# Kernel optimization log

Hardware: AMD Instinct MI355X
Metric: run time of the kernel (lower is better)

Reference implementation:

```python
import jax, jax.numpy as jnp
import numpy as np

E, H, I, T = 8, 2048, 1024, 16384  # experts, hidden, moe_intermediate, total tokens


def setup_inputs() -> dict:
    key = jax.random.key(0)
    k1, k2, k3, k4 = jax.random.split(key, 4)
    hidden_states = jax.random.normal(k1, (T, H), dtype=jnp.float32)
    # ragged per-expert token counts, summing exactly to T (tokens pre-sorted by expert)
    group_sizes = jnp.array([1024, 3072, 2048, 4096, 512, 1536, 2560, 1536], dtype=jnp.int32)
    std = 0.01  # nn.initializers.normal() default stddev
    gate_w = jax.random.normal(k2, (E, H, I), dtype=jnp.float32) * std
    up_w = jax.random.normal(k3, (E, H, I), dtype=jnp.float32) * std
    down_w = jax.random.normal(k4, (E, I, H), dtype=jnp.float32) * std
    return {"hidden_states": hidden_states, "gate_w": gate_w, "up_w": up_w,
            "down_w": down_w, "group_sizes": group_sizes}


def reference(hidden_states, gate_w, up_w, down_w, group_sizes):
    # grouped GEMM: rows of hidden_states are contiguous per-expert blocks of
    # sizes group_sizes[e]; each block is multiplied by that expert's kernel.
    g = jax.lax.ragged_dot(hidden_states, gate_w, group_sizes)   # [T, I]
    u = jax.lax.ragged_dot(hidden_states, up_w, group_sizes)     # [T, I]
    h = jax.nn.silu(g) * u                                       # SwiGLU gating
    return jax.lax.ragged_dot(h, down_w, group_sizes)            # [T, H]
```

## Files before the change

kernel.cpp:

```cpp
#include <hip/hip_runtime.h>
#include <hip/hip_bf16.h>

#define E_ 8
#define H_ 2048
#define I_ 1024
#define T_ 16384
#define BM 128
#define BN 128
#define BK 64
#define MAX_MT 136

typedef __bf16 bf16x8 __attribute__((ext_vector_type(8)));
typedef float f32x4 __attribute__((ext_vector_type(4)));

__device__ __forceinline__ unsigned short f2bf(float f) {
  unsigned int x = __float_as_uint(f);
  x += 0x7FFFu + ((x >> 16) & 1u);
  return (unsigned short)(x >> 16);
}

__device__ __forceinline__ void gl_lds16(const void* g, void* s) {
  __builtin_amdgcn_global_load_lds(
      (const __attribute__((address_space(1))) void*)g,
      (__attribute__((address_space(3))) void*)s, 16, 0, 0);
}

__device__ __forceinline__ void sync_full() {
  __builtin_amdgcn_s_waitcnt(0);
  __syncthreads();
}

__device__ __forceinline__ bool find_tile(const int* gs, int tile, int& e,
                                          int& row0, int& rowEnd) {
  int base = 0, tb = 0;
  e = -1;
  for (int i = 0; i < E_; i++) {
    int g = gs[i];
    int nt = (g + BM - 1) >> 7;
    if (e < 0 && tile < tb + nt) {
      e = i;
      row0 = base + (tile - tb) * BM;
      rowEnd = base + g;
    }
    tb += nt;
    base += g;
  }
  return e >= 0;
}


__global__ void cvt_hs(const float* __restrict__ in, ushort* __restrict__ out) {
  size_t i = ((size_t)blockIdx.x * 256 + threadIdx.x) * 8;
  float4 a = *(const float4*)(in + i);
  float4 b = *(const float4*)(in + i + 4);
  union { ushort u[8]; uint4 v; } p;
  p.u[0] = f2bf(a.x); p.u[1] = f2bf(a.y); p.u[2] = f2bf(a.z); p.u[3] = f2bf(a.w);
  p.u[4] = f2bf(b.x); p.u[5] = f2bf(b.y); p.u[6] = f2bf(b.z); p.u[7] = f2bf(b.w);
  *(uint4*)(out + i) = p.v;
}

__global__ void cvt_tr(const float* __restrict__ in, ushort* __restrict__ out,
                       int K, int N) {
  __shared__ ushort tile[64][65];
  int n0 = blockIdx.x * 64, k0 = blockIdx.y * 64;
  const float* src = in + (size_t)blockIdx.z * K * N;
  ushort* dst = out + (size_t)blockIdx.z * K * N;
  int t = threadIdx.x;
  int rb = t >> 4, c4 = (t & 15) * 4;
#pragma unroll
  for (int i = 0; i < 4; i++) {
    int r = rb + i * 16;
    float4 v = *(const float4*)(src + (size_t)(k0 + r) * N + n0 + c4);
    tile[r][c4 + 0] = f2bf(v.x);
    tile[r][c4 + 1] = f2bf(v.y);
    tile[r][c4 + 2] = f2bf(v.z);
    tile[r][c4 + 3] = f2bf(v.w);
  }
  __syncthreads();
#pragma unroll
  for (int i = 0; i < 2; i++) {
    int c = t + i * 256;
    int n = c >> 3, kc = c & 7;
    union { ushort u[8]; uint4 v; } p;
#pragma unroll
    for (int j = 0; j < 8; j++) p.u[j] = tile[kc * 8 + j][n];
    *(uint4*)(dst + (size_t)(n0 + n) * K + k0 + kc * 8) = p.v;
  }
}

__global__ __launch_bounds__(256, 2) void gemm_gateup(
    const ushort* __restrict__ A, const ushort* __restrict__ BgT,
    const ushort* __restrict__ BuT, const int* __restrict__ gs,
    ushort* __restrict__ Hb) {
  __shared__ __align__(16) ushort sA[BM * BK];
  __shared__ __align__(16) ushort sG[BN * BK];
  __shared__ __align__(16) ushort sU[BN * BK];

  int e, row0, rowEnd;
  if (!find_tile(gs, blockIdx.x, e, row0, rowEnd)) return;
  const int n0 = blockIdx.y * BN;

  const int t = threadIdx.x;
  const int lane = t & 63;
  const int w = t >> 6;
  const int wm = w & 1, wn = w >> 1;

  int offAB[4];
  int offA[4];
#pragma unroll
  for (int i = 0; i < 4; i++) {
    int c = i * 256 + t;
    int r = c >> 3;
    int kcs = (c & 7) ^ (r & 7);
    offAB[i] = r * H_ + kcs * 8;
    int ar = row0 + r; if (ar > T_ - 1) ar = T_ - 1;
    offA[i] = ar * H_ + kcs * 8;
  }
  const ushort* pA = A;
  const ushort* pG = BgT + ((size_t)e * I_ + n0) * H_;
  const ushort* pU = BuT + ((size_t)e * I_ + n0) * H_;
  const int ldst = w * 64 * 8;

  const int l15 = lane & 15, l7 = lane & 7, lk = lane >> 4;
  const int sw0 = (lk ^ l7) * 8;
  const int sw1 = ((lk + 4) ^ l7) * 8;
  const ushort* aF0 = sA + (wm * 64 + l15) * BK + sw0;
  const ushort* aF1 = sA + (wm * 64 + l15) * BK + sw1;
  const ushort* gF0 = sG + (wn * 64 + l15) * BK + sw0;
  const ushort* gF1 = sG + (wn * 64 + l15) * BK + sw1;
  const ushort* uF0 = sU + (wn * 64 + l15) * BK + sw0;
  const ushort* uF1 = sU + (wn * 64 + l15) * BK + sw1;

  f32x4 accG[4][4], accU[4][4];
#pragma unroll
  for (int mi = 0; mi < 4; mi++)
#pragma unroll
    for (int ni = 0; ni < 4; ni++) {
      accG[mi][ni] = (f32x4){0.f, 0.f, 0.f, 0.f};
      accU[mi][ni] = (f32x4){0.f, 0.f, 0.f, 0.f};
    }

  for (int k0 = 0; k0 < H_; k0 += BK) {
#pragma unroll
    for (int i = 0; i < 4; i++) {
      gl_lds16(pA + offA[i],  sA + i * 2048 + ldst);
      gl_lds16(pG + offAB[i], sG + i * 2048 + ldst);
      gl_lds16(pU + offAB[i], sU + i * 2048 + ldst);
    }
    pA += BK; pG += BK; pU += BK;
    sync_full();

#pragma unroll
    for (int ks = 0; ks < 2; ks++) {
      bf16x8 af[4], gf[4], uf[4];
#pragma unroll
      for (int i = 0; i < 4; i++) {
        af[i] = *(const bf16x8*)((ks ? aF1 : aF0) + i * 16 * BK);
        gf[i] = *(const bf16x8*)((ks ? gF1 : gF0) + i * 16 * BK);
        uf[i] = *(const bf16x8*)((ks ? uF1 : uF0) + i * 16 * BK);
      }
#pragma unroll
      for (int mi = 0; mi < 4; mi++)
#pragma unroll
        for (int ni = 0; ni < 4; ni++) {
          accG[mi][ni] = __builtin_amdgcn_mfma_f32_16x16x32_bf16(af[mi], gf[ni], accG[mi][ni], 0, 0, 0);
          accU[mi][ni] = __builtin_amdgcn_mfma_f32_16x16x32_bf16(af[mi], uf[ni], accU[mi][ni], 0, 0, 0);
        }
    }
    sync_full();
  }

  const int crow = row0 + wm * 64 + ((lane >> 4) << 2);
  const int ccol = n0 + wn * 64 + (lane & 15);
#pragma unroll
  for (int mi = 0; mi < 4; mi++)
#pragma unroll
    for (int ni = 0; ni < 4; ni++)
#pragma unroll
      for (int r = 0; r < 4; r++) {
        int row = crow + mi * 16 + r;
        if (row < rowEnd) {
          float g = accG[mi][ni][r];
          float u = accU[mi][ni][r];
          float h = (g / (1.0f + __expf(-g))) * u;
          Hb[(size_t)row * I_ + ccol + ni * 16] = f2bf(h);
        }
      }
}

__global__ __launch_bounds__(256, 3) void gemm_down(
    const ushort* __restrict__ A, const ushort* __restrict__ BdT,
    const int* __restrict__ gs, float* __restrict__ Out) {
  __shared__ __align__(16) ushort sA[BM * BK];
  __shared__ __align__(16) ushort sB[BN * BK];

  int e, row0, rowEnd;
  if (!find_tile(gs, blockIdx.x, e, row0, rowEnd)) return;
  const int n0 = blockIdx.y * BN;

  const int t = threadIdx.x;
  const int lane = t & 63;
  const int w = t >> 6;
  const int wm = w & 1, wn = w >> 1;

  int offB[4], offA[4];
#pragma unroll
  for (int i = 0; i < 4; i++) {
    int c = i * 256 + t;
    int r = c >> 3;
    int kcs = (c & 7) ^ (r & 7);
    offB[i] = r * I_ + kcs * 8;
    int ar = row0 + r; if (ar > T_ - 1) ar = T_ - 1;
    offA[i] = ar * I_ + kcs * 8;
  }
  const ushort* pA = A;
  const ushort* pB = BdT + ((size_t)e * H_ + n0) * I_;
  const int ldst = w * 64 * 8;

  const int l15 = lane & 15, l7 = lane & 7, lk = lane >> 4;
  const int sw0 = (lk ^ l7) * 8;
  const int sw1 = ((lk + 4) ^ l7) * 8;
  const ushort* aF0 = sA + (wm * 64 + l15) * BK + sw0;
  const ushort* aF1 = sA + (wm * 64 + l15) * BK + sw1;
  const ushort* bF0 = sB + (wn * 64 + l15) * BK + sw0;
  const ushort* bF1 = sB + (wn * 64 + l15) * BK + sw1;

  f32x4 acc[4][4];
#pragma unroll
  for (int mi = 0; mi < 4; mi++)
#pragma unroll
    for (int ni = 0; ni < 4; ni++) acc[mi][ni] = (f32x4){0.f, 0.f, 0.f, 0.f};

  for (int k0 = 0; k0 < I_; k0 += BK) {
#pragma unroll
    for (int i = 0; i < 4; i++) {
      gl_lds16(pA + offA[i], sA + i * 2048 + ldst);
      gl_lds16(pB + offB[i], sB + i * 2048 + ldst);
    }
    pA += BK; pB += BK;
    sync_full();

#pragma unroll
    for (int ks = 0; ks < 2; ks++) {
      bf16x8 af[4], bf[4];
#pragma unroll
      for (int i = 0; i < 4; i++) {
        af[i] = *(const bf16x8*)((ks ? aF1 : aF0) + i * 16 * BK);
        bf[i] = *(const bf16x8*)((ks ? bF1 : bF0) + i * 16 * BK);
      }
#pragma unroll
      for (int mi = 0; mi < 4; mi++)
#pragma unroll
        for (int ni = 0; ni < 4; ni++)
          acc[mi][ni] = __builtin_amdgcn_mfma_f32_16x16x32_bf16(af[mi], bf[ni], acc[mi][ni], 0, 0, 0);
    }
    sync_full();
  }

  const int crow = row0 + wm * 64 + ((lane >> 4) << 2);
  const int ccol = n0 + wn * 64 + (lane & 15);
#pragma unroll
  for (int mi = 0; mi < 4; mi++)
#pragma unroll
    for (int ni = 0; ni < 4; ni++)
#pragma unroll
      for (int r = 0; r < 4; r++) {
        int row = crow + mi * 16 + r;
        if (row < rowEnd) Out[(size_t)row * H_ + ccol + ni * 16] = acc[mi][ni][r];
      }
}

extern "C" void kernel_launch(void* const* d_in, const int* in_sizes, int n_in,
                              void* d_out, int out_size, void* d_ws, size_t ws_size,
                              hipStream_t stream) {
  const float* hs = (const float*)d_in[0];
  const float* gw = (const float*)d_in[1];
  const float* uw = (const float*)d_in[2];
  const float* dw = (const float*)d_in[3];
  const int* gs = (const int*)d_in[4];
  float* out = (float*)d_out;

  ushort* hsb = (ushort*)d_ws;
  ushort* wgT = hsb + (size_t)T_ * H_;
  ushort* wuT = wgT + (size_t)E_ * H_ * I_;
  ushort* wdT = wuT + (size_t)E_ * H_ * I_;
  ushort* hb  = wdT + (size_t)E_ * H_ * I_;

  cvt_hs<<<((size_t)T_ * H_) / (256 * 8), 256, 0, stream>>>(hs, hsb);
  cvt_tr<<<dim3(I_ / 64, H_ / 64, E_), 256, 0, stream>>>(gw, wgT, H_, I_);
  cvt_tr<<<dim3(I_ / 64, H_ / 64, E_), 256, 0, stream>>>(uw, wuT, H_, I_);
  cvt_tr<<<dim3(H_ / 64, I_ / 64, E_), 256, 0, stream>>>(dw, wdT, I_, H_);

  gemm_gateup<<<dim3(MAX_MT, I_ / BN), 256, 0, stream>>>(hsb, wgT, wuT, gs, hb);
  gemm_down<<<dim3(MAX_MT, H_ / BN), 256, 0, stream>>>(hb, wdT, gs, out);
}
```

Before: 613.1 us.

## Double-buffer LDS with 256-row tiles, 8 waves, interleaved prefetch and MFMA

Both grouped GEMM kernels move to 256-row M tiles with 512 threads and a 128 KB dynamic LDS double buffer. Each K step is split into four phases that prefetch the next tile's sub-blocks through global_load_lds while MFMAs run on the current slot, using partial vmcnt waits instead of full waitcnt+syncthreads. s_setprio raises priority around the MFMA bursts. This targets load latency and per-step barrier cost and raises operand reuse per LDS byte, at the cost of fewer, larger tiles, more padding waste on ragged groups, and lower occupancy from the large LDS footprint.

```diff
diff --git a/kernel.cpp b/kernel.cpp
--- a/kernel.cpp
+++ b/kernel.cpp
@@ -5,10 +5,10 @@
 #define H_ 2048
 #define I_ 1024
 #define T_ 16384
-#define BM 128
-#define BN 128
 #define BK 64
-#define MAX_MT 136
+#define BM 256
+#define MT_ (T_ / BM + E_)
+#define SLOT 32768
 
 typedef __bf16 bf16x8 __attribute__((ext_vector_type(8)));
 typedef float f32x4 __attribute__((ext_vector_type(4)));
@@ -25,10 +25,23 @@
       (__attribute__((address_space(3))) void*)s, 16, 0, 0);
 }
 
-__device__ __forceinline__ void sync_full() {
-  __builtin_amdgcn_s_waitcnt(0);
-  __syncthreads();
-}
+#define VMCNT4 asm volatile("s_waitcnt vmcnt(4)" ::: "memory")
+#define BARRIER                      \
+  do {                               \
+    __builtin_amdgcn_s_barrier();    \
+    __builtin_amdgcn_sched_barrier(0); \
+  } while (0)
+
+#define MFMA16(ACC, AF, BF)                                                     \
+  do {                                                                          \
+    __builtin_amdgcn_s_setprio(1);                                              \
+    _Pragma("unroll") for (int ks = 0; ks < 2; ks++)                            \
+    _Pragma("unroll") for (int mi = 0; mi < 4; mi++)                            \
+    _Pragma("unroll") for (int ni = 0; ni < 2; ni++)                            \
+      ACC[mi][ni] = __builtin_amdgcn_mfma_f32_16x16x32_bf16(                    \
+          AF[mi][ks], BF[ni][ks], ACC[mi][ni], 0, 0, 0);                        \
+    __builtin_amdgcn_s_setprio(0);                                              \
+  } while (0)
 
 __device__ __forceinline__ bool find_tile(const int* gs, int tile, int& e,
                                           int& row0, int& rowEnd) {
@@ -36,7 +49,7 @@
   e = -1;
   for (int i = 0; i < E_; i++) {
     int g = gs[i];
-    int nt = (g + BM - 1) >> 7;
+    int nt = (g + BM - 1) >> 8;
     if (e < 0 && tile < tb + nt) {
       e = i;
       row0 = base + (tile - tb) * BM;
@@ -88,186 +101,249 @@
   }
 }
 
-__global__ __launch_bounds__(256, 2) void gemm_gateup(
+__global__ __launch_bounds__(512, 2) void gemm_gateup(
     const ushort* __restrict__ A, const ushort* __restrict__ BgT,
     const ushort* __restrict__ BuT, const int* __restrict__ gs,
     ushort* __restrict__ Hb) {
-  __shared__ __align__(16) ushort sA[BM * BK];
-  __shared__ __align__(16) ushort sG[BN * BK];
-  __shared__ __align__(16) ushort sU[BN * BK];
+  extern __shared__ __align__(16) ushort ls[];
 
   int e, row0, rowEnd;
   if (!find_tile(gs, blockIdx.x, e, row0, rowEnd)) return;
-  const int n0 = blockIdx.y * BN;
+  const int n0 = blockIdx.y * 128;
 
   const int t = threadIdx.x;
   const int lane = t & 63;
   const int w = t >> 6;
   const int wm = w & 1, wn = w >> 1;
-
-  int offAB[4];
-  int offA[4];
-#pragma unroll
-  for (int i = 0; i < 4; i++) {
-    int c = i * 256 + t;
-    int r = c >> 3;
-    int kcs = (c & 7) ^ (r & 7);
-    offAB[i] = r * H_ + kcs * 8;
-    int ar = row0 + r; if (ar > T_ - 1) ar = T_ - 1;
-    offA[i] = ar * H_ + kcs * 8;
-  }
-  const ushort* pA = A;
-  const ushort* pG = BgT + ((size_t)e * I_ + n0) * H_;
-  const ushort* pU = BuT + ((size_t)e * I_ + n0) * H_;
-  const int ldst = w * 64 * 8;
+  const int ldW = w * 512;
+
+  int oAlo[2], oAhi[2], oB[2];
+#pragma unroll
+  for (int l = 0; l < 2; l++) {
+    int c = l * 512 + t;
+    int r = c >> 3, kc = (c & 7) ^ (r & 7);
+    int a0 = row0 + r;       if (a0 > T_ - 1) a0 = T_ - 1;
+    int a1 = row0 + 128 + r; if (a1 > T_ - 1) a1 = T_ - 1;
+    oAlo[l] = a0 * H_ + kc * 8;
+    oAhi[l] = a1 * H_ + kc * 8;
+    oB[l] = (e * I_ + n0 + r) * H_ + kc * 8;
+  }
 
   const int l15 = lane & 15, l7 = lane & 7, lk = lane >> 4;
-  const int sw0 = (lk ^ l7) * 8;
-  const int sw1 = ((lk + 4) ^ l7) * 8;
-  const ushort* aF0 = sA + (wm * 64 + l15) * BK + sw0;
-  const ushort* aF1 = sA + (wm * 64 + l15) * BK + sw1;
-  const ushort* gF0 = sG + (wn * 64 + l15) * BK + sw0;
-  const ushort* gF1 = sG + (wn * 64 + l15) * BK + sw1;
-  const ushort* uF0 = sU + (wn * 64 + l15) * BK + sw0;
-  const ushort* uF1 = sU + (wn * 64 + l15) * BK + sw1;
-
-  f32x4 accG[4][4], accU[4][4];
+  const int s0 = (lk ^ l7) * 8, s1 = ((lk + 4) ^ l7) * 8;
+  const int arow = (wm * 64 + l15) * 64;
+  const int brow = (wn * 32 + l15) * 64;
+
+  f32x4 accG0[4][2], accG1[4][2], accU0[4][2], accU1[4][2];
 #pragma unroll
   for (int mi = 0; mi < 4; mi++)
 #pragma unroll
-    for (int ni = 0; ni < 4; ni++) {
-      accG[mi][ni] = (f32x4){0.f, 0.f, 0.f, 0.f};
-      accU[mi][ni] = (f32x4){0.f, 0.f, 0.f, 0.f};
-    }
-
-  for (int k0 = 0; k0 < H_; k0 += BK) {
-#pragma unroll
-    for (int i = 0; i < 4; i++) {
-      gl_lds16(pA + offA[i],  sA + i * 2048 + ldst);
-      gl_lds16(pG + offAB[i], sG + i * 2048 + ldst);
-      gl_lds16(pU + offAB[i], sU + i * 2048 + ldst);
-    }
-    pA += BK; pG += BK; pU += BK;
-    sync_full();
-
-#pragma unroll
-    for (int ks = 0; ks < 2; ks++) {
-      bf16x8 af[4], gf[4], uf[4];
-#pragma unroll
-      for (int i = 0; i < 4; i++) {
-        af[i] = *(const bf16x8*)((ks ? aF1 : aF0) + i * 16 * BK);
-        gf[i] = *(const bf16x8*)((ks ? gF1 : gF0) + i * 16 * BK);
-        uf[i] = *(const bf16x8*)((ks ? uF1 : uF0) + i * 16 * BK);
-      }
-#pragma unroll
-      for (int mi = 0; mi < 4; mi++)
-#pragma unroll
-        for (int ni = 0; ni < 4; ni++) {
-          accG[mi][ni] = __builtin_amdgcn_mfma_f32_16x16x32_bf16(af[mi], gf[ni], accG[mi][ni], 0, 0, 0);
-          accU[mi][ni] = __builtin_amdgcn_mfma_f32_16x16x32_bf16(af[mi], uf[ni], accU[mi][ni], 0, 0, 0);
+    for (int ni = 0; ni < 2; ni++) {
+      accG0[mi][ni] = (f32x4){0.f, 0.f, 0.f, 0.f};
+      accG1[mi][ni] = (f32x4){0.f, 0.f, 0.f, 0.f};
+      accU0[mi][ni] = (f32x4){0.f, 0.f, 0.f, 0.f};
+      accU1[mi][ni] = (f32x4){0.f, 0.f, 0.f, 0.f};
+    }
+
+  gl_lds16(A + oAlo[0], ls + 0 + ldW);
+  gl_lds16(A + oAlo[1], ls + 4096 + ldW);
+  gl_lds16(BgT + oB[0], ls + 16384 + ldW);
+  gl_lds16(BgT + oB[1], ls + 16384 + 4096 + ldW);
+  gl_lds16(BuT + oB[0], ls + 24576 + ldW);
+  gl_lds16(BuT + oB[1], ls + 24576 + 4096 + ldW);
+  gl_lds16(A + oAhi[0], ls + 8192 + ldW);
+  gl_lds16(A + oAhi[1], ls + 8192 + 4096 + ldW);
+
+#pragma unroll 2
+  for (int tt = 0; tt < H_ / BK; tt++) {
+    const int p = tt & 1, q = p ^ 1;
+    const ushort* sa = ls + p * SLOT;
+    ushort* sq = ls + q * SLOT;
+    const int kn = (tt + 1 < H_ / BK ? tt + 1 : tt) * BK;
+    bf16x8 af[4][2], gf[2][2], uf[2][2];
+
+    VMCNT4; BARRIER;
+    gl_lds16(A + oAlo[0] + kn, sq + 0 + ldW);
+    gl_lds16(A + oAlo[1] + kn, sq + 4096 + ldW);
+#pragma unroll
+    for (int mi = 0; mi < 4; mi++) {
+      af[mi][0] = *(const bf16x8*)(sa + arow + mi * 1024 + s0);
+      af[mi][1] = *(const bf16x8*)(sa + arow + mi * 1024 + s1);
+    }
+#pragma unroll
+    for (int ni = 0; ni < 2; ni++) {
+      gf[ni][0] = *(const bf16x8*)(sa + 16384 + brow + ni * 1024 + s0);
+      gf[ni][1] = *(const bf16x8*)(sa + 16384 + brow + ni * 1024 + s1);
+    }
+    MFMA16(accG0, af, gf);
+
+    VMCNT4; BARRIER;
+    gl_lds16(BgT + oB[0] + kn, sq + 16384 + ldW);
+    gl_lds16(BgT + oB[1] + kn, sq + 16384 + 4096 + ldW);
+#pragma unroll
+    for (int ni = 0; ni < 2; ni++) {
+      uf[ni][0] = *(const bf16x8*)(sa + 24576 + brow + ni * 1024 + s0);
+      uf[ni][1] = *(const bf16x8*)(sa + 24576 + brow + ni * 1024 + s1);
+    }
+    MFMA16(accU0, af, uf);
+
+    VMCNT4; BARRIER;
+    gl_lds16(BuT + oB[0] + kn, sq + 24576 + ldW);
+    gl_lds16(BuT + oB[1] + kn, sq + 24576 + 4096 + ldW);
+#pragma unroll
+    for (int mi = 0; mi < 4; mi++) {
+      af[mi][0] = *(const bf16x8*)(sa + 8192 + arow + mi * 1024 + s0);
+      af[mi][1] = *(const bf16x8*)(sa + 8192 + arow + mi * 1024 + s1);
+    }
+    MFMA16(accG1, af, gf);
+
+    BARRIER;
+    gl_lds16(A + oAhi[0] + kn, sq + 8192 + ldW);
+    gl_lds16(A + oAhi[1] + kn, sq + 8192 + 4096 + ldW);
+    MFMA16(accU1, af, uf);
+  }
+
+  const int cr = row0 + wm * 64 + (lk << 2);
+  const int cc = n0 + wn * 32 + l15;
+#pragma unroll
+  for (int mh = 0; mh < 2; mh++)
+#pragma unroll
+    for (int mi = 0; mi < 4; mi++)
+#pragma unroll
+      for (int ni = 0; ni < 2; ni++)
+#pragma unroll
+        for (int r = 0; r < 4; r++) {
+          int row = cr + mh * 128 + mi * 16 + r;
+          if (row < rowEnd) {
+            float g = mh ? accG1[mi][ni][r] : accG0[mi][ni][r];
+            float u = mh ? accU1[mi][ni][r] : accU0[mi][ni][r];
+            float h = (g / (1.0f + __expf(-g))) * u;
+            Hb[(size_t)row * I_ + cc + ni * 16] = f2bf(h);
+          }
         }
-    }
-    sync_full();
-  }
-
-  const int crow = row0 + wm * 64 + ((lane >> 4) << 2);
-  const int ccol = n0 + wn * 64 + (lane & 15);
-#pragma unroll
-  for (int mi = 0; mi < 4; mi++)
-#pragma unroll
-    for (int ni = 0; ni < 4; ni++)
-#pragma unroll
-      for (int r = 0; r < 4; r++) {
-        int row = crow + mi * 16 + r;
-        if (row < rowEnd) {
-          float g = accG[mi][ni][r];
-          float u = accU[mi][ni][r];
-          float h = (g / (1.0f + __expf(-g))) * u;
-          Hb[(size_t)row * I_ + ccol + ni * 16] = f2bf(h);
-        }
-      }
-}
-
-__global__ __launch_bounds__(256, 3) void gemm_down(
+}
+
+__global__ __launch_bounds__(512, 2) void gemm_down(
     const ushort* __restrict__ A, const ushort* __restrict__ BdT,
     const int* __restrict__ gs, float* __restrict__ Out) {
-  __shared__ __align__(16) ushort sA[BM * BK];
-  __shared__ __align__(16) ushort sB[BN * BK];
+  extern __shared__ __align__(16) ushort ls[];
 
   int e, row0, rowEnd;
   if (!find_tile(gs, blockIdx.x, e, row0, rowEnd)) return;
-  const int n0 = blockIdx.y * BN;
+  const int n0 = blockIdx.y * 256;
 
   const int t = threadIdx.x;
   const int lane = t & 63;
   const int w = t >> 6;
   const int wm = w & 1, wn = w >> 1;
-
-  int offB[4], offA[4];
-#pragma unroll
-  for (int i = 0; i < 4; i++) {
-    int c = i * 256 + t;
-    int r = c >> 3;
-    int kcs = (c & 7) ^ (r & 7);
-    offB[i] = r * I_ + kcs * 8;
-    int ar = row0 + r; if (ar > T_ - 1) ar = T_ - 1;
-    offA[i] = ar * I_ + kcs * 8;
-  }
-  const ushort* pA = A;
-  const ushort* pB = BdT + ((size_t)e * H_ + n0) * I_;
-  const int ldst = w * 64 * 8;
+  const int ldW = w * 512;
+
+  int oAlo[2], oAhi[2], oBlo[2], oBhi[2];
+#pragma unroll
+  for (int l = 0; l < 2; l++) {
+    int c = l * 512 + t;
+    int r = c >> 3, kc = (c & 7) ^ (r & 7);
+    int a0 = row0 + r;       if (a0 > T_ - 1) a0 = T_ - 1;
+    int a1 = row0 + 128 + r; if (a1 > T_ - 1) a1 = T_ - 1;
+    oAlo[l] = a0 * I_ + kc * 8;
+    oAhi[l] = a1 * I_ + kc * 8;
+    oBlo[l] = (e * H_ + n0 + r) * I_ + kc * 8;
+    oBhi[l] = (e * H_ + n0 + 128 + r) * I_ + kc * 8;
+  }
 
   const int l15 = lane & 15, l7 = lane & 7, lk = lane >> 4;
-  const int sw0 = (lk ^ l7) * 8;
-  const int sw1 = ((lk + 4) ^ l7) * 8;
-  const ushort* aF0 = sA + (wm * 64 + l15) * BK + sw0;
-  const ushort* aF1 = sA + (wm * 64 + l15) * BK + sw1;
-  const ushort* bF0 = sB + (wn * 64 + l15) * BK + sw0;
-  const ushort* bF1 = sB + (wn * 64 + l15) * BK + sw1;
-
-  f32x4 acc[4][4];
+  const int s0 = (lk ^ l7) * 8, s1 = ((lk + 4) ^ l7) * 8;
+  const int arow = (wm * 64 + l15) * 64;
+  const int brow = (wn * 32 + l15) * 64;
+
+  f32x4 acc00[4][2], acc01[4][2], acc11[4][2], acc10[4][2];
 #pragma unroll
   for (int mi = 0; mi < 4; mi++)
 #pragma unroll
-    for (int ni = 0; ni < 4; ni++) acc[mi][ni] = (f32x4){0.f, 0.f, 0.f, 0.f};
-
-  for (int k0 = 0; k0 < I_; k0 += BK) {
-#pragma unroll
-    for (int i = 0; i < 4; i++) {
-      gl_lds16(pA + offA[i], sA + i * 2048 + ldst);
-      gl_lds16(pB + offB[i], sB + i * 2048 + ldst);
-    }
-    pA += BK; pB += BK;
-    sync_full();
-
-#pragma unroll
-    for (int ks = 0; ks < 2; ks++) {
-      bf16x8 af[4], bf[4];
-#pragma unroll
-      for (int i = 0; i < 4; i++) {
-        af[i] = *(const bf16x8*)((ks ? aF1 : aF0) + i * 16 * BK);
-        bf[i] = *(const bf16x8*)((ks ? bF1 : bF0) + i * 16 * BK);
-      }
-#pragma unroll
-      for (int mi = 0; mi < 4; mi++)
-#pragma unroll
-        for (int ni = 0; ni < 4; ni++)
-          acc[mi][ni] = __builtin_amdgcn_mfma_f32_16x16x32_bf16(af[mi], bf[ni], acc[mi][ni], 0, 0, 0);
-    }
-    sync_full();
-  }
-
-  const int crow = row0 + wm * 64 + ((lane >> 4) << 2);
-  const int ccol = n0 + wn * 64 + (lane & 15);
-#pragma unroll
-  for (int mi = 0; mi < 4; mi++)
-#pragma unroll
-    for (int ni = 0; ni < 4; ni++)
-#pragma unroll
-      for (int r = 0; r < 4; r++) {
-        int row = crow + mi * 16 + r;
-        if (row < rowEnd) Out[(size_t)row * H_ + ccol + ni * 16] = acc[mi][ni][r];
-      }
+    for (int ni = 0; ni < 2; ni++) {
+      acc00[mi][ni] = (f32x4){0.f, 0.f, 0.f, 0.f};
+      acc01[mi][ni] = (f32x4){0.f, 0.f, 0.f, 0.f};
+      acc11[mi][ni] = (f32x4){0.f, 0.f, 0.f, 0.f};
+      acc10[mi][ni] = (f32x4){0.f, 0.f, 0.f, 0.f};
+    }
+
+  gl_lds16(A + oAlo[0], ls + 0 + ldW);
+  gl_lds16(A + oAlo[1], ls + 4096 + ldW);
+  gl_lds16(BdT + oBlo[0], ls + 16384 + ldW);
+  gl_lds16(BdT + oBlo[1], ls + 16384 + 4096 + ldW);
+  gl_lds16(BdT + oBhi[0], ls + 24576 + ldW);
+  gl_lds16(BdT + oBhi[1], ls + 24576 + 4096 + ldW);
+  gl_lds16(A + oAhi[0], ls + 8192 + ldW);
+  gl_lds16(A + oAhi[1], ls + 8192 + 4096 + ldW);
+
+#pragma unroll 2
+  for (int tt = 0; tt < I_ / BK; tt++) {
+    const int p = tt & 1, q = p ^ 1;
+    const ushort* sa = ls + p * SLOT;
+    ushort* sq = ls + q * SLOT;
+    const int kn = (tt + 1 < I_ / BK ? tt + 1 : tt) * BK;
+    bf16x8 af[4][2], bf0[2][2], bf1[2][2];
+
+    VMCNT4; BARRIER;
+    gl_lds16(A + oAlo[0] + kn, sq + 0 + ldW);
+    gl_lds16(A + oAlo[1] + kn, sq + 4096 + ldW);
+#pragma unroll
+    for (int mi = 0; mi < 4; mi++) {
+      af[mi][0] = *(const bf16x8*)(sa + arow + mi * 1024 + s0);
+      af[mi][1] = *(const bf16x8*)(sa + arow + mi * 1024 + s1);
+    }
+#pragma unroll
+    for (int ni = 0; ni < 2; ni++) {
+      bf0[ni][0] = *(const bf16x8*)(sa + 16384 + brow + ni * 1024 + s0);
+      bf0[ni][1] = *(const bf16x8*)(sa + 16384 + brow + ni * 1024 + s1);
+    }
+    MFMA16(acc00, af, bf0);
+
+    VMCNT4; BARRIER;
+    gl_lds16(BdT + oBlo[0] + kn, sq + 16384 + ldW);
+    gl_lds16(BdT + oBlo[1] + kn, sq + 16384 + 4096 + ldW);
+#pragma unroll
+    for (int ni = 0; ni < 2; ni++) {
+      bf1[ni][0] = *(const bf16x8*)(sa + 16384 + 8192 + brow + ni * 1024 + s0);
+      bf1[ni][1] = *(const bf16x8*)(sa + 16384 + 8192 + brow + ni * 1024 + s1);
+    }
+    MFMA16(acc01, af, bf1);
+
+    VMCNT4; BARRIER;
+    gl_lds16(BdT + oBhi[0] + kn, sq + 24576 + ldW);
+    gl_lds16(BdT + oBhi[1] + kn, sq + 24576 + 4096 + ldW);
+#pragma unroll
+    for (int mi = 0; mi < 4; mi++) {
+      af[mi][0] = *(const bf16x8*)(sa + 8192 + arow + mi * 1024 + s0);
+      af[mi][1] = *(const bf16x8*)(sa + 8192 + arow + mi * 1024 + s1);
+    }
+    MFMA16(acc11, af, bf1);
+
+    BARRIER;
+    gl_lds16(A + oAhi[0] + kn, sq + 8192 + ldW);
+    gl_lds16(A + oAhi[1] + kn, sq + 8192 + 4096 + ldW);
+    MFMA16(acc10, af, bf0);
+  }
+
+  const int cr = row0 + wm * 64 + (lk << 2);
+  const int cc = n0 + wn * 32 + l15;
+#pragma unroll
+  for (int mh = 0; mh < 2; mh++)
+#pragma unroll
+    for (int mi = 0; mi < 4; mi++)
+#pragma unroll
+      for (int nh = 0; nh < 2; nh++)
+#pragma unroll
+        for (int ni = 0; ni < 2; ni++)
+#pragma unroll
+          for (int r = 0; r < 4; r++) {
+            int row = cr + mh * 128 + mi * 16 + r;
+            if (row < rowEnd) {
+              float v = mh ? (nh ? acc11[mi][ni][r] : acc10[mi][ni][r])
+                           : (nh ? acc01[mi][ni][r] : acc00[mi][ni][r]);
+              Out[(size_t)row * H_ + cc + nh * 128 + ni * 16] = v;
+            }
+          }
 }
 
 extern "C" void kernel_launch(void* const* d_in, const int* in_sizes, int n_in,
@@ -286,11 +362,16 @@
   ushort* wdT = wuT + (size_t)E_ * H_ * I_;
   ushort* hb  = wdT + (size_t)E_ * H_ * I_;
 
+  (void)hipFuncSetAttribute(reinterpret_cast<const void*>(gemm_gateup),
+                            hipFuncAttributeMaxDynamicSharedMemorySize, 131072);
+  (void)hipFuncSetAttribute(reinterpret_cast<const void*>(gemm_down),
+                            hipFuncAttributeMaxDynamicSharedMemorySize, 131072);
+
   cvt_hs<<<((size_t)T_ * H_) / (256 * 8), 256, 0, stream>>>(hs, hsb);
   cvt_tr<<<dim3(I_ / 64, H_ / 64, E_), 256, 0, stream>>>(gw, wgT, H_, I_);
   cvt_tr<<<dim3(I_ / 64, H_ / 64, E_), 256, 0, stream>>>(uw, wuT, H_, I_);
   cvt_tr<<<dim3(H_ / 64, I_ / 64, E_), 256, 0, stream>>>(dw, wdT, I_, H_);
 
-  gemm_gateup<<<dim3(MAX_MT, I_ / BN), 256, 0, stream>>>(hsb, wgT, wuT, gs, hb);
-  gemm_down<<<dim3(MAX_MT, H_ / BN), 256, 0, stream>>>(hb, wdT, gs, out);
-}
+  gemm_gateup<<<dim3(MT_, I_ / 128), 512, 131072, stream>>>(hsb, wgT, wuT, gs, hb);
+  gemm_down<<<dim3(MT_, H_ / 256), 512, 131072, stream>>>(hb, wdT, gs, out);
+}
```

New measurement: 546.0 us. -10.9%, faster.

## Rework grouped GEMMs into 512-thread, 3-stage pipelined kernels with larger M tiles

Applied to the files above, without the earlier changes.

Both grouped GEMM kernels now use 256-row M tiles, 512 threads (8 waves) and BK=32. Global-to-LDS loads go through a triple-buffered dynamic shared memory ring, using partial vmcnt waits and a single barrier per step instead of a full drain twice per K step. MFMA sections are raised with setprio. The last tile is shifted to stay in bounds, and rows outside the group are masked on store. The aim is to overlap loads with MFMA compute and cut synchronisation overhead, at the cost of more LDS per block, lower occupancy and wasted rows on partial tiles.

```diff
diff --git a/kernel.cpp b/kernel.cpp
--- a/kernel.cpp
+++ b/kernel.cpp
@@ -5,10 +5,9 @@
 #define H_ 2048
 #define I_ 1024
 #define T_ 16384
-#define BM 128
-#define BN 128
-#define BK 64
-#define MAX_MT 136
+#define BM 256
+#define MT_ (T_ / BM + E_)
+#define SLOTU 12288
 
 typedef __bf16 bf16x8 __attribute__((ext_vector_type(8)));
 typedef float f32x4 __attribute__((ext_vector_type(4)));
@@ -25,10 +24,12 @@
       (__attribute__((address_space(3))) void*)s, 16, 0, 0);
 }
 
-__device__ __forceinline__ void sync_full() {
-  __builtin_amdgcn_s_waitcnt(0);
-  __syncthreads();
-}
+#define VMCNT3 asm volatile("s_waitcnt vmcnt(3)" ::: "memory")
+#define BAR                            \
+  do {                                 \
+    __builtin_amdgcn_s_barrier();      \
+    __builtin_amdgcn_sched_barrier(0); \
+  } while (0)
 
 __device__ __forceinline__ bool find_tile(const int* gs, int tile, int& e,
                                           int& row0, int& rowEnd) {
@@ -36,7 +37,7 @@
   e = -1;
   for (int i = 0; i < E_; i++) {
     int g = gs[i];
-    int nt = (g + BM - 1) >> 7;
+    int nt = (g + BM - 1) >> 8;
     if (e < 0 && tile < tb + nt) {
       e = i;
       row0 = base + (tile - tb) * BM;
@@ -88,142 +89,135 @@
   }
 }
 
-__global__ __launch_bounds__(256, 2) void gemm_gateup(
+__global__ __launch_bounds__(512, 4) void gemm_gateup(
     const ushort* __restrict__ A, const ushort* __restrict__ BgT,
     const ushort* __restrict__ BuT, const int* __restrict__ gs,
     ushort* __restrict__ Hb) {
-  __shared__ __align__(16) ushort sA[BM * BK];
-  __shared__ __align__(16) ushort sG[BN * BK];
-  __shared__ __align__(16) ushort sU[BN * BK];
+  extern __shared__ __align__(16) ushort ls[];
 
   int e, row0, rowEnd;
   if (!find_tile(gs, blockIdx.x, e, row0, rowEnd)) return;
-  const int n0 = blockIdx.y * BN;
+  const int n0 = blockIdx.y * 64;
 
   const int t = threadIdx.x;
   const int lane = t & 63;
   const int w = t >> 6;
-  const int wm = w & 1, wn = w >> 1;
-
-  int offAB[4];
-  int offA[4];
-#pragma unroll
-  for (int i = 0; i < 4; i++) {
-    int c = i * 256 + t;
-    int r = c >> 3;
-    int kcs = (c & 7) ^ (r & 7);
-    offAB[i] = r * H_ + kcs * 8;
-    int ar = row0 + r; if (ar > T_ - 1) ar = T_ - 1;
-    offA[i] = ar * H_ + kcs * 8;
-  }
-  const ushort* pA = A;
-  const ushort* pG = BgT + ((size_t)e * I_ + n0) * H_;
-  const ushort* pU = BuT + ((size_t)e * I_ + n0) * H_;
-  const int ldst = w * 64 * 8;
-
-  const int l15 = lane & 15, l7 = lane & 7, lk = lane >> 4;
-  const int sw0 = (lk ^ l7) * 8;
-  const int sw1 = ((lk + 4) ^ l7) * 8;
-  const ushort* aF0 = sA + (wm * 64 + l15) * BK + sw0;
-  const ushort* aF1 = sA + (wm * 64 + l15) * BK + sw1;
-  const ushort* gF0 = sG + (wn * 64 + l15) * BK + sw0;
-  const ushort* gF1 = sG + (wn * 64 + l15) * BK + sw1;
-  const ushort* uF0 = sU + (wn * 64 + l15) * BK + sw0;
-  const ushort* uF1 = sU + (wn * 64 + l15) * BK + sw1;
-
-  f32x4 accG[4][4], accU[4][4];
+  const int wm = w & 3, wn = w >> 2;
+
+  const int cr = t >> 2;
+  const int sw8 = ((t & 3) ^ (cr & 3)) * 8;
+  const int voff = cr * H_ + sw8;
+  const int dA0 = t * 8, dA1 = 4096 + t * 8, dGU = 8192 + t * 8;
+
+  const int rowB = (row0 > T_ - BM) ? (T_ - BM) : row0;
+  const ushort* bA0 = A + (size_t)rowB * H_;
+  const ushort* bA1 = bA0 + (size_t)128 * H_;
+  const ushort* bGU = (w < 4) ? BgT + (size_t)(e * I_ + n0) * H_
+                              : BuT + (size_t)(e * I_ + n0) * H_ - (size_t)64 * H_;
+
+  const int l15 = lane & 15, lk = lane >> 4;
+  const int pl = l15 * 32 + (lk ^ (l15 & 3)) * 8;
+  const int aoff = wm * 2048 + pl;
+  const int boff = 8192 + wn * 1024 + pl;
+
+  f32x4 accG[4][2], accU[4][2];
 #pragma unroll
   for (int mi = 0; mi < 4; mi++)
 #pragma unroll
-    for (int ni = 0; ni < 4; ni++) {
+    for (int ni = 0; ni < 2; ni++) {
       accG[mi][ni] = (f32x4){0.f, 0.f, 0.f, 0.f};
       accU[mi][ni] = (f32x4){0.f, 0.f, 0.f, 0.f};
     }
 
-  for (int k0 = 0; k0 < H_; k0 += BK) {
-#pragma unroll
-    for (int i = 0; i < 4; i++) {
-      gl_lds16(pA + offA[i],  sA + i * 2048 + ldst);
-      gl_lds16(pG + offAB[i], sG + i * 2048 + ldst);
-      gl_lds16(pU + offAB[i], sU + i * 2048 + ldst);
+#pragma unroll
+  for (int tp = 0; tp < 2; tp++) {
+    ushort* sq = ls + tp * SLOTU;
+    gl_lds16(bA0 + voff + tp * 32, sq + dA0);
+    gl_lds16(bA1 + voff + tp * 32, sq + dA1);
+    gl_lds16(bGU + voff + tp * 32, sq + dGU);
+  }
+
+#pragma unroll 3
+  for (int tt = 0; tt < H_ / 32; tt++) {
+    const ushort* sa = ls + (tt % 3) * SLOTU;
+    ushort* sq = ls + ((tt + 2) % 3) * SLOTU;
+    int t2 = tt + 2; if (t2 > H_ / 32 - 1) t2 = H_ / 32 - 1;
+    const int kn = t2 * 32;
+
+    VMCNT3;
+    BAR;
+
+    gl_lds16(bA0 + voff + kn, sq + dA0);
+    gl_lds16(bA1 + voff + kn, sq + dA1);
+    gl_lds16(bGU + voff + kn, sq + dGU);
+
+    bf16x8 af[4], gf[2], uf[2];
+#pragma unroll
+    for (int mi = 0; mi < 4; mi++)
+      af[mi] = *(const bf16x8*)(sa + aoff + mi * 512);
+#pragma unroll
+    for (int ni = 0; ni < 2; ni++) {
+      gf[ni] = *(const bf16x8*)(sa + boff + ni * 512);
+      uf[ni] = *(const bf16x8*)(sa + boff + 2048 + ni * 512);
     }
-    pA += BK; pG += BK; pU += BK;
-    sync_full();
-
-#pragma unroll
-    for (int ks = 0; ks < 2; ks++) {
-      bf16x8 af[4], gf[4], uf[4];
-#pragma unroll
-      for (int i = 0; i < 4; i++) {
-        af[i] = *(const bf16x8*)((ks ? aF1 : aF0) + i * 16 * BK);
-        gf[i] = *(const bf16x8*)((ks ? gF1 : gF0) + i * 16 * BK);
-        uf[i] = *(const bf16x8*)((ks ? uF1 : uF0) + i * 16 * BK);
+
+    __builtin_amdgcn_s_setprio(1);
+#pragma unroll
+    for (int mi = 0; mi < 4; mi++)
+#pragma unroll
+      for (int ni = 0; ni < 2; ni++) {
+        accG[mi][ni] = __builtin_amdgcn_mfma_f32_16x16x32_bf16(af[mi], gf[ni], accG[mi][ni], 0, 0, 0);
+        accU[mi][ni] = __builtin_amdgcn_mfma_f32_16x16x32_bf16(af[mi], uf[ni], accU[mi][ni], 0, 0, 0);
       }
-#pragma unroll
-      for (int mi = 0; mi < 4; mi++)
-#pragma unroll
-        for (int ni = 0; ni < 4; ni++) {
-          accG[mi][ni] = __builtin_amdgcn_mfma_f32_16x16x32_bf16(af[mi], gf[ni], accG[mi][ni], 0, 0, 0);
-          accU[mi][ni] = __builtin_amdgcn_mfma_f32_16x16x32_bf16(af[mi], uf[ni], accU[mi][ni], 0, 0, 0);
-        }
-    }
-    sync_full();
-  }
-
-  const int crow = row0 + wm * 64 + ((lane >> 4) << 2);
-  const int ccol = n0 + wn * 64 + (lane & 15);
+    __builtin_amdgcn_s_setprio(0);
+  }
+
+  const int orow = rowB + wm * 64 + lk * 4;
+  const int ocol = n0 + wn * 32 + l15;
 #pragma unroll
   for (int mi = 0; mi < 4; mi++)
 #pragma unroll
-    for (int ni = 0; ni < 4; ni++)
+    for (int ni = 0; ni < 2; ni++)
 #pragma unroll
       for (int r = 0; r < 4; r++) {
-        int row = crow + mi * 16 + r;
-        if (row < rowEnd) {
+        int row = orow + mi * 16 + r;
+        if (row >= row0 && row < rowEnd) {
           float g = accG[mi][ni][r];
           float u = accU[mi][ni][r];
           float h = (g / (1.0f + __expf(-g))) * u;
-          Hb[(size_t)row * I_ + ccol + ni * 16] = f2bf(h);
+          Hb[(size_t)row * I_ + ocol + ni * 16] = f2bf(h);
         }
       }
 }
 
-__global__ __launch_bounds__(256, 3) void gemm_down(
+__global__ __launch_bounds__(512, 4) void gemm_down(
     const ushort* __restrict__ A, const ushort* __restrict__ BdT,
     const int* __restrict__ gs, float* __restrict__ Out) {
-  __shared__ __align__(16) ushort sA[BM * BK];
-  __shared__ __align__(16) ushort sB[BN * BK];
+  extern __shared__ __align__(16) ushort ls[];
 
   int e, row0, rowEnd;
   if (!find_tile(gs, blockIdx.x, e, row0, rowEnd)) return;
-  const int n0 = blockIdx.y * BN;
+  const int n0 = blockIdx.y * 128;
 
   const int t = threadIdx.x;
   const int lane = t & 63;
   const int w = t >> 6;
-  const int wm = w & 1, wn = w >> 1;
-
-  int offB[4], offA[4];
-#pragma unroll
-  for (int i = 0; i < 4; i++) {
-    int c = i * 256 + t;
-    int r = c >> 3;
-    int kcs = (c & 7) ^ (r & 7);
-    offB[i] = r * I_ + kcs * 8;
-    int ar = row0 + r; if (ar > T_ - 1) ar = T_ - 1;
-    offA[i] = ar * I_ + kcs * 8;
-  }
-  const ushort* pA = A;
-  const ushort* pB = BdT + ((size_t)e * H_ + n0) * I_;
-  const int ldst = w * 64 * 8;
-
-  const int l15 = lane & 15, l7 = lane & 7, lk = lane >> 4;
-  const int sw0 = (lk ^ l7) * 8;
-  const int sw1 = ((lk + 4) ^ l7) * 8;
-  const ushort* aF0 = sA + (wm * 64 + l15) * BK + sw0;
-  const ushort* aF1 = sA + (wm * 64 + l15) * BK + sw1;
-  const ushort* bF0 = sB + (wn * 64 + l15) * BK + sw0;
-  const ushort* bF1 = sB + (wn * 64 + l15) * BK + sw1;
+  const int wm = w & 3, wn = w >> 2;
+
+  const int cr = t >> 2;
+  const int sw8 = ((t & 3) ^ (cr & 3)) * 8;
+  const int voff = cr * I_ + sw8;
+  const int dA0 = t * 8, dA1 = 4096 + t * 8, dB = 8192 + t * 8;
+
+  const int rowB = (row0 > T_ - BM) ? (T_ - BM) : row0;
+  const ushort* bA0 = A + (size_t)rowB * I_;
+  const ushort* bA1 = bA0 + (size_t)128 * I_;
+  const ushort* bB = BdT + (size_t)(e * H_ + n0) * I_;
+
+  const int l15 = lane & 15, lk = lane >> 4;
+  const int pl = l15 * 32 + (lk ^ (l15 & 3)) * 8;
+  const int aoff = wm * 2048 + pl;
+  const int boff = 8192 + wn * 2048 + pl;
 
   f32x4 acc[4][4];
 #pragma unroll
@@ -231,42 +225,55 @@
 #pragma unroll
     for (int ni = 0; ni < 4; ni++) acc[mi][ni] = (f32x4){0.f, 0.f, 0.f, 0.f};
 
-  for (int k0 = 0; k0 < I_; k0 += BK) {
-#pragma unroll
-    for (int i = 0; i < 4; i++) {
-      gl_lds16(pA + offA[i], sA + i * 2048 + ldst);
-      gl_lds16(pB + offB[i], sB + i * 2048 + ldst);
-    }
-    pA += BK; pB += BK;
-    sync_full();
-
-#pragma unroll
-    for (int ks = 0; ks < 2; ks++) {
-      bf16x8 af[4], bf[4];
-#pragma unroll
-      for (int i = 0; i < 4; i++) {
-        af[i] = *(const bf16x8*)((ks ? aF1 : aF0) + i * 16 * BK);
-        bf[i] = *(const bf16x8*)((ks ? bF1 : bF0) + i * 16 * BK);
-      }
-#pragma unroll
-      for (int mi = 0; mi < 4; mi++)
-#pragma unroll
-        for (int ni = 0; ni < 4; ni++)
-          acc[mi][ni] = __builtin_amdgcn_mfma_f32_16x16x32_bf16(af[mi], bf[ni], acc[mi][ni], 0, 0, 0);
-    }
-    sync_full();
-  }
-
-  const int crow = row0 + wm * 64 + ((lane >> 4) << 2);
-  const int ccol = n0 + wn * 64 + (lane & 15);
+#pragma unroll
+  for (int tp = 0; tp < 2; tp++) {
+    ushort* sq = ls + tp * SLOTU;
+    gl_lds16(bA0 + voff + tp * 32, sq + dA0);
+    gl_lds16(bA1 + voff + tp * 32, sq + dA1);
+    gl_lds16(bB + voff + tp * 32, sq + dB);
+  }
+
+#pragma unroll 3
+  for (int tt = 0; tt < I_ / 32; tt++) {
+    const ushort* sa = ls + (tt % 3) * SLOTU;
+    ushort* sq = ls + ((tt + 2) % 3) * SLOTU;
+    int t2 = tt + 2; if (t2 > I_ / 32 - 1) t2 = I_ / 32 - 1;
+    const int kn = t2 * 32;
+
+    VMCNT3; BAR;
+
+    gl_lds16(bA0 + voff + kn, sq + dA0);
+    gl_lds16(bA1 + voff + kn, sq + dA1);
+    gl_lds16(bB + voff + kn, sq + dB);
+
+    bf16x8 af[4], bf[4];
+#pragma unroll
+    for (int mi = 0; mi < 4; mi++)
+      af[mi] = *(const bf16x8*)(sa + aoff + mi * 512);
+#pragma unroll
+    for (int ni = 0; ni < 4; ni++)
+      bf[ni] = *(const bf16x8*)(sa + boff + ni * 512);
+
+    __builtin_amdgcn_s_setprio(1);
+#pragma unroll
+    for (int mi = 0; mi < 4; mi++)
+#pragma unroll
+      for (int ni = 0; ni < 4; ni++)
+        acc[mi][ni] = __builtin_amdgcn_mfma_f32_16x16x32_bf16(af[mi], bf[ni], acc[mi][ni], 0, 0, 0);
+    __builtin_amdgcn_s_setprio(0);
+  }
+
+  const int orow = rowB + wm * 64 + lk * 4;
+  const int ocol = n0 + wn * 64 + l15;
 #pragma unroll
   for (int mi = 0; mi < 4; mi++)
 #pragma unroll
     for (int ni = 0; ni < 4; ni++)
 #pragma unroll
       for (int r = 0; r < 4; r++) {
-        int row = crow + mi * 16 + r;
-        if (row < rowEnd) Out[(size_t)row * H_ + ccol + ni * 16] = acc[mi][ni][r];
+        int row = orow + mi * 16 + r;
+        if (row >= row0 && row < rowEnd)
+          Out[(size_t)row * H_ + ocol + ni * 16] = acc[mi][ni][r];
       }
 }
 
@@ -286,11 +293,16 @@
   ushort* wdT = wuT + (size_t)E_ * H_ * I_;
   ushort* hb  = wdT + (size_t)E_ * H_ * I_;
 
+  (void)hipFuncSetAttribute(reinterpret_cast<const void*>(gemm_gateup),
+                            hipFuncAttributeMaxDynamicSharedMemorySize, 73728);
+  (void)hipFuncSetAttribute(reinterpret_cast<const void*>(gemm_down),
+                            hipFuncAttributeMaxDynamicSharedMemorySize, 73728);
+
   cvt_hs<<<((size_t)T_ * H_) / (256 * 8), 256, 0, stream>>>(hs, hsb);
   cvt_tr<<<dim3(I_ / 64, H_ / 64, E_), 256, 0, stream>>>(gw, wgT, H_, I_);
   cvt_tr<<<dim3(I_ / 64, H_ / 64, E_), 256, 0, stream>>>(uw, wuT, H_, I_);
   cvt_tr<<<dim3(H_ / 64, I_ / 64, E_), 256, 0, stream>>>(dw, wdT, I_, H_);
 
-  gemm_gateup<<<dim3(MAX_MT, I_ / BN), 256, 0, stream>>>(hsb, wgT, wuT, gs, hb);
-  gemm_down<<<dim3(MAX_MT, H_ / BN), 256, 0, stream>>>(hb, wdT, gs, out);
-}
+  gemm_gateup<<<dim3(MT_, I_ / 64), 512, 73728, stream>>>(hsb, wgT, wuT, gs, hb);
+  gemm_down<<<dim3(MT_, H_ / 128), 512, 73728, stream>>>(hb, wdT, gs, out);
+}
```

New measurement: 617.5 us. Within noise of the previous version (+0.7%).
